# Optimization experiments

Measured on AMD Instinct MI355X. Metric: run time of the kernel, lower is better.

Reference implementation:

```python
import jax, jax.numpy as jnp
import numpy as np

EPSILON = 0.01
N_ITERS = 100
EPS_STAB = 1e-08
KERNEL_CLAMP = 50.0


def _cost_matrix(x, y):
    # squared euclidean distances, (n, m)
    x2 = jnp.sum(x * x, axis=1, keepdims=True)          # (n,1)
    y2 = jnp.sum(y * y, axis=1, keepdims=True).T        # (1,m)
    c = x2 + y2 - 2.0 * (x @ y.T)
    c = jnp.maximum(c, 0.0)  # numerical guard, matches cdist(p=2)**2 >= 0
    return jnp.nan_to_num(c, nan=0.0, posinf=1e6, neginf=0.0)


def _sinkhorn_cost(X, Y):
    n, m = X.shape[0], Y.shape[0]
    C = _cost_matrix(X, Y)
    scaled = jnp.clip(-C / EPSILON, -KERNEL_CLAMP, 0.0)
    K = jnp.maximum(jnp.nan_to_num(jnp.exp(scaled), nan=0.0, posinf=0.0, neginf=0.0), EPS_STAB)
    a = jnp.full((n,), 1.0 / n, dtype=C.dtype)
    b = jnp.full((m,), 1.0 / m, dtype=C.dtype)
    u0 = jnp.ones_like(a)
    v0 = jnp.ones_like(b)

    def body(_, uv):
        u, v = uv
        Kv = jnp.maximum(K @ v, EPS_STAB)
        u = a / Kv
        Ktu = jnp.maximum(K.T @ u, EPS_STAB)
        v = b / Ktu
        return (u, v)

    u, v = jax.lax.fori_loop(0, N_ITERS, body, (u0, v0))
    # cost = sum(u_i * K_ij * v_j * C_ij)
    cost = u @ ((K * C) @ v)
    return jnp.maximum(cost, 0.0)


def setup_inputs() -> dict:
    key = jax.random.key(0)
    k1, k2 = jax.random.split(key)
    X = jax.random.normal(k1, (8192, 128), dtype=jnp.float32)
    Y = jax.random.normal(k2, (8192, 128), dtype=jnp.float32)
    return {"X": X, "Y": Y}


def reference(X, Y):
    ot_xy = _sinkhorn_cost(X, Y)
    ot_xx = _sinkhorn_cost(X, jax.lax.stop_gradient(X))
    ot_yy = _sinkhorn_cost(Y, jax.lax.stop_gradient(Y))
    divergence = ot_xy - 0.5 * (ot_xx + ot_yy)
    return jnp.clip(divergence, 0.0, 10000.0)
```

## Files before the change

kernel.cpp:

```cpp
#include <hip/hip_runtime.h>
#include <math.h>

#define NROW 8192
#define DDIM 128
#define DP 32
#define CAP 16384
#define NITERS 100
#define NWARM 6
#define AC (1.0f / 8192.0f)
#define LSTRIDE2 40

struct Entry { int i, j; float s, t; };


typedef __attribute__((ext_vector_type(8))) short frag_ab;
typedef __attribute__((ext_vector_type(4))) float frag_cd;

__device__ inline unsigned short f2bf(float f) {
    unsigned u = __float_as_uint(f);
    return (unsigned short)((u + 0x7FFFu + ((u >> 16) & 1u)) >> 16);
}

__global__ void norms_k(const float* __restrict__ X, const float* __restrict__ Y,
                        float* __restrict__ x2, float* __restrict__ y2,
                        float* __restrict__ x2p, float* __restrict__ y2p,
                        unsigned short* __restrict__ Xbf, unsigned short* __restrict__ Ybf,
                        int* counts, double* accum, Entry* lists) {
    int idx = blockIdx.x * 256 + threadIdx.x;
    if (idx < 3) counts[idx] = NROW;
    else if (idx < 8) counts[idx] = 0;
    if (idx < 3 * 264) accum[idx] = 0.0;
    if (idx < 3 * NROW) {
        int p = idx >> 13, i = idx & (NROW - 1);
        Entry e; e.i = i; e.j = i; e.s = 0.f; e.t = 0.f;
        lists[(size_t)p * CAP + i] = e;
    }
    int gw = idx >> 6;
    int lane = threadIdx.x & 63;
    if (gw >= 2 * NROW) return;
    const float* M = (gw < NROW) ? X : Y;
    float* out = (gw < NROW) ? x2 : y2;
    float* outp = (gw < NROW) ? x2p : y2p;
    unsigned short* Mb = (gw < NROW) ? Xbf : Ybf;
    int r = (gw < NROW) ? gw : gw - NROW;
    float2 v = *(const float2*)(M + (size_t)r * DDIM + lane * 2);
    if (lane < 16) {
        unsigned pk = (unsigned)f2bf(v.x) | ((unsigned)f2bf(v.y) << 16);
        *(unsigned*)(Mb + (size_t)r * DP + lane * 2) = pk;
    }
    float s = v.x * v.x + v.y * v.y;
    float sp = (lane < 16) ? s : 0.f;
    for (int o = 32; o; o >>= 1) s += __shfl_down(s, o, 64);
    for (int o = 8; o; o >>= 1) sp += __shfl_down(sp, o, 64);
    if (lane == 0) { out[r] = s; outp[r] = sp; }
}

__global__ __launch_bounds__(256) void scan_k(const unsigned short* __restrict__ Xbf,
                                              const unsigned short* __restrict__ Ybf,
                                              const float* __restrict__ x2p,
                                              const float* __restrict__ y2p,
                                              int* counts, Entry* lists) {
    int bid = blockIdx.x;
    int p, bx, by;
    if (bid < 4096) { p = 0; by = bid >> 6; bx = bid & 63; }
    else {
        int r = bid - 4096;
        p = 1 + (r >= 2080);
        int q = r - (p == 2) * 2080;
        int a = (int)((129.0f - sqrtf((float)(16641 - 8 * q))) * 0.5f);
        while (a * 64 - ((a * (a - 1)) >> 1) > q) a--;
        while ((a + 1) * 64 - (((a + 1) * a) >> 1) <= q) a++;
        bx = a;
        by = a + (q - (a * 64 - ((a * (a - 1)) >> 1)));
    }
    const unsigned short* Ab = (p == 2) ? Ybf : Xbf;
    const unsigned short* Bb = (p == 0) ? Ybf : ((p == 1) ? Xbf : Ybf);
    const float* na = (p == 2) ? y2p : x2p;
    const float* nb = (p == 0) ? y2p : ((p == 1) ? x2p : y2p);
    int i0 = bx * 128, j0 = by * 128;

    __shared__ unsigned short As[128 * LSTRIDE2];
    __shared__ unsigned short Bs[128 * LSTRIDE2];
    __shared__ float sMinA[32];
    int t = threadIdx.x;

    const unsigned short* ga = Ab + (size_t)i0 * DP;
    const unsigned short* gb = Bb + (size_t)j0 * DP;
    #pragma unroll
    for (int c = 0; c < 2; c++) {
        int u = c * 256 + t;
        int row = u >> 2, col = (u & 3) * 8;
        uint4 wa = *(const uint4*)(ga + u * 8);
        uint4 wb = *(const uint4*)(gb + u * 8);
        *(uint4*)&As[row * LSTRIDE2 + col] = wa;
        *(uint4*)&Bs[row * LSTRIDE2 + col] = wb;
    }
    if (t < 32) {
        const float* nn = na + i0 + t * 4;
        sMinA[t] = fminf(fminf(nn[0], nn[1]), fminf(nn[2], nn[3]));
    }
    __syncthreads();

    int w = t >> 6, lane = t & 63;
    int lm = lane & 15, quad = lane >> 4;
    int wr = (w & 1) * 64, wc = (w >> 1) * 64;

    frag_cd acc[4][4];
    #pragma unroll
    for (int rt = 0; rt < 4; rt++)
        #pragma unroll
        for (int ct = 0; ct < 4; ct++) acc[rt][ct] = (frag_cd){0.f, 0.f, 0.f, 0.f};

    int abase = (wr + lm) * LSTRIDE2 + quad * 8;
    int bbase = (wc + lm) * LSTRIDE2 + quad * 8;
    {
        frag_ab a[4], b[4];
        #pragma unroll
        for (int rt = 0; rt < 4; rt++) a[rt] = *(const frag_ab*)&As[abase + rt * 16 * LSTRIDE2];
        #pragma unroll
        for (int ct = 0; ct < 4; ct++) b[ct] = *(const frag_ab*)&Bs[bbase + ct * 16 * LSTRIDE2];
        #pragma unroll
        for (int rt = 0; rt < 4; rt++)
            #pragma unroll
            for (int ct = 0; ct < 4; ct++)
                acc[rt][ct] = __builtin_amdgcn_mfma_f32_16x16x32_bf16(a[rt], b[ct], acc[rt][ct], 0, 0, 0);
    }

    Entry* list = lists + (size_t)p * CAP;
    float yj_[4];
    #pragma unroll
    for (int ct = 0; ct < 4; ct++) yj_[ct] = nb[j0 + wc + ct * 16 + lm];
    float minyj = fminf(fminf(yj_[0], yj_[1]), fminf(yj_[2], yj_[3]));

    #pragma unroll
    for (int rt = 0; rt < 4; rt++) {
        float m0 = fmaxf(fmaxf(acc[rt][0][0], acc[rt][0][1]), fmaxf(acc[rt][0][2], acc[rt][0][3]));
        float m1 = fmaxf(fmaxf(acc[rt][1][0], acc[rt][1][1]), fmaxf(acc[rt][1][2], acc[rt][1][3]));
        float m2 = fmaxf(fmaxf(acc[rt][2][0], acc[rt][2][1]), fmaxf(acc[rt][2][2], acc[rt][2][3]));
        float m3 = fmaxf(fmaxf(acc[rt][3][0], acc[rt][3][1]), fmaxf(acc[rt][3][2], acc[rt][3][3]));
        float mx = fmaxf(fmaxf(m0, m1), fmaxf(m2, m3));
        float mna = sMinA[(wr >> 2) + rt * 4 + quad];
        if (mna + minyj - 2.f * mx < 2.0f) {
            #pragma unroll
            for (int ct = 0; ct < 4; ct++) {
                int j = j0 + wc + ct * 16 + lm;
                float yj = yj_[ct];
                #pragma unroll
                for (int reg = 0; reg < 4; reg++) {
                    int i = i0 + wr + rt * 16 + quad * 4 + reg;
                    float Ct = na[i] + yj - 2.f * acc[rt][ct][reg];
                    if (Ct < 2.0f && i != j) {
                        if (p == 0) {
                            int idx = atomicAdd(&counts[0], 1);
                            if (idx < CAP) { Entry e; e.i = i; e.j = j; e.s = 0.f; e.t = 0.f; list[idx] = e; }
                        } else if (i < j) {
                            int idx = atomicAdd(&counts[p], 2);
                            if (idx < CAP) { Entry e; e.i = i; e.j = j; e.s = 0.f; e.t = 0.f; list[idx] = e; }
                            if (idx + 1 < CAP) { Entry e; e.i = j; e.j = i; e.s = 0.f; e.t = 0.f; list[idx + 1] = e; }
                        }
                    }
                }
            }
        }
    }
}

__global__ __launch_bounds__(256) void exact_k(const float* __restrict__ X,
                                               const float* __restrict__ Y,
                                               const float* __restrict__ x2,
                                               const float* __restrict__ y2,
                                               int* counts, Entry* lists,
                                               float* __restrict__ sdiag,
                                               float* __restrict__ tdiag) {
    int p = blockIdx.y;
    const float* A = (p == 2) ? Y : X;
    const float* B = (p == 0) ? Y : ((p == 1) ? X : Y);
    const float* na = (p == 2) ? y2 : x2;
    const float* nb = (p == 0) ? y2 : ((p == 1) ? x2 : y2);
    int cnt = counts[p]; if (cnt > CAP) cnt = CAP;
    Entry* list = lists + (size_t)p * CAP;
    int w = (blockIdx.x * 256 + threadIdx.x) >> 6;
    int lane = threadIdx.x & 63;
    for (int e = w; e < cnt; e += 8192) {
        int i = list[e].i, j = list[e].j;
        const float* ar = A + (size_t)i * DDIM;
        const float* br = B + (size_t)j * DDIM;
        float dot = ar[lane] * br[lane] + ar[lane + 64] * br[lane + 64];
        for (int o = 32; o; o >>= 1) dot += __shfl_down(dot, o, 64);
        if (lane == 0) {
            float raw = na[i] + nb[j] - 2.0f * dot;
            float C = fmaxf(raw, 0.0f);
            float sc = fmaxf(-C * 100.0f, -50.0f);
            float K = fmaxf(expf(sc), 1e-8f);
            float s = K - 1e-8f;
            float tv = (raw >= 0.f) ? s * C : (-1e-8f) * raw;
            list[e].s = s;
            list[e].t = tv;
            if (i == j) {
                sdiag[p * NROW + i] = s;
                tdiag[p * NROW + i] = tv;
            } else if (s != 0.f || tv != 0.f) {
                atomicAdd(&counts[3 + p], 1);
            }
        }
    }
}

__global__ __launch_bounds__(1024, 1) void sink2_k(const int* counts,
                                                   const Entry* __restrict__ lists,
                                                   const float* __restrict__ sdiag,
                                                   float* __restrict__ u_g,
                                                   float* __restrict__ v_g,
                                                   double* accum) {
    int p = blockIdx.x;
    const Entry* list = lists + (size_t)p * CAP;
    int cnt = counts[p]; if (cnt > CAP) cnt = CAP;
    int nres = counts[3 + p];
    double* acc = accum + (size_t)p * 264;
    float* up = u_g + (size_t)p * NROW;
    float* vp = v_g + (size_t)p * NROW;

    __shared__ float u_s[NROW];
    __shared__ float v_s[NROW];
    __shared__ float redS[2][16];
    __shared__ unsigned redC[16];
    int t = threadIdx.x;
    int wid = t >> 6, lane = t & 63;

    if (nres == 0) {
        float vk[8], uk[8], sk[8];
        unsigned pv2[8];
        #pragma unroll
        for (int k = 0; k < 8; k++) {
            sk[k] = sdiag[p * NROW + t + 1024 * k];
            vk[k] = 1.0f; uk[k] = AC; pv2[k] = 0xFFFFFFFFu;
        }
        unsigned flags = 3u;
        int par = 0, last = 0, done = 0;
        float bu_last = 0.f;
        for (int it = 0; it < NWARM; it++) {
            float s = 0.f;
            #pragma unroll
            for (int k = 0; k < 8; k++) s += vk[k];
            for (int o = 32; o; o >>= 1) s += __shfl_down(s, o, 64);
            if (lane == 0) { redS[par][wid] = s; redC[wid] = flags; }
            __syncthreads();
            float sumv = 0.f; unsigned anyf = 0;
            #pragma unroll
            for (int w2 = 0; w2 < 16; w2++) { sumv += redS[par][w2]; anyf |= redC[w2]; }
            par ^= 1;
            if (it > 0) {
                if (!(anyf & 1)) { done = 1; break; }
                if (!(anyf & 2)) {
                    if (((NITERS - it) & 1) == 0) { done = 1; break; }
                    last = 1;
                }
            }
            float base = 1e-8f * sumv;
            #pragma unroll
            for (int k = 0; k < 8; k++) {
                float kv = fmaxf(base + sk[k] * vk[k], 1e-8f);
                uk[k] = AC * __builtin_amdgcn_rcpf(kv);
            }
            s = 0.f;
            #pragma unroll
            for (int k = 0; k < 8; k++) s += uk[k];
            for (int o = 32; o; o >>= 1) s += __shfl_down(s, o, 64);
            if (lane == 0) redS[par][wid] = s;
            __syncthreads();
            float sumu = 0.f;
            #pragma unroll
            for (int w2 = 0; w2 < 16; w2++) sumu += redS[par][w2];
            par ^= 1;
            base = 1e-8f * sumu;
            bu_last = base;
            unsigned d1 = 0, d2 = 0;
            #pragma unroll
            for (int k = 0; k < 8; k++) {
                float kv = fmaxf(base + sk[k] * uk[k], 1e-8f);
                float nv = AC * __builtin_amdgcn_rcpf(kv);
                unsigned nb_ = __float_as_uint(nv);
                d1 |= nb_ ^ __float_as_uint(vk[k]);
                d2 |= nb_ ^ pv2[k];
                pv2[k] = __float_as_uint(vk[k]);
                vk[k] = nv;
            }
            flags = (__any(d1 != 0) ? 1u : 0u) | (__any(d2 != 0) ? 2u : 0u);
            if (last) { done = 1; break; }
        }
        float bv_f = 0.f;
        int R = 0;
        if (!done) {
            float s = 0.f;
            #pragma unroll
            for (int k = 0; k < 8; k++) s += vk[k];
            for (int o = 32; o; o >>= 1) s += __shfl_down(s, o, 64);
            if (lane == 0) redS[par][wid] = s;
            __syncthreads();
            float sumv = 0.f;
            #pragma unroll
            for (int w2 = 0; w2 < 16; w2++) sumv += redS[par][w2];
            bv_f = 1e-8f * sumv;
            R = NITERS - NWARM;
        }
        #pragma unroll
        for (int k = 0; k < 8; k++) {
            int i = t + 1024 * k;
            up[i] = uk[k]; vp[i] = vk[k];
        }
        if (t == 0) { acc[5] = (double)R; acc[6] = (double)bu_last; acc[7] = (double)bv_f; }
    } else {
        for (int i = t; i < NROW; i += 1024) { u_s[i] = 1.0f; v_s[i] = 1.0f; }
        __syncthreads();
        for (int it = 0; it < NITERS; it++) {
            {
                float sv = 0.f;
                for (int i = t; i < NROW; i += 1024) sv += v_s[i];
                for (int o = 32; o; o >>= 1) sv += __shfl_down(sv, o, 64);
                if (lane == 0) u_s[wid] = sv;
                __syncthreads();
                if (t < 64) {
                    float s2 = (t < 16) ? u_s[t] : 0.f;
                    for (int o = 8; o; o >>= 1) s2 += __shfl_down(s2, o, 64);
                    if (t == 0) u_s[0] = s2;
                }
                __syncthreads();
                float sum_v = u_s[0];
                __syncthreads();
                for (int i = t; i < NROW; i += 1024) u_s[i] = 1e-8f * sum_v;
                __syncthreads();
                for (int e = t; e < cnt; e += 1024)
                    atomicAdd(&u_s[list[e].i], list[e].s * v_s[list[e].j]);
                __syncthreads();
                for (int i = t; i < NROW; i += 1024) u_s[i] = AC / fmaxf(u_s[i], 1e-8f);
                __syncthreads();
            }
            {
                float su = 0.f;
                for (int i = t; i < NROW; i += 1024) su += u_s[i];
                for (int o = 32; o; o >>= 1) su += __shfl_down(su, o, 64);
                if (lane == 0) v_s[wid] = su;
                __syncthreads();
                if (t < 64) {
                    float s2 = (t < 16) ? v_s[t] : 0.f;
                    for (int o = 8; o; o >>= 1) s2 += __shfl_down(s2, o, 64);
                    if (t == 0) v_s[0] = s2;
                }
                __syncthreads();
                float sum_u = v_s[0];
                __syncthreads();
                for (int i = t; i < NROW; i += 1024) v_s[i] = 1e-8f * sum_u;
                __syncthreads();
                for (int e = t; e < cnt; e += 1024)
                    atomicAdd(&v_s[list[e].j], list[e].s * u_s[list[e].i]);
                __syncthreads();
                for (int i = t; i < NROW; i += 1024) v_s[i] = AC / fmaxf(v_s[i], 1e-8f);
                __syncthreads();
            }
        }
        for (int i = t; i < NROW; i += 1024) { up[i] = u_s[i]; vp[i] = v_s[i]; }
        if (t == 0) { acc[5] = 0.0; acc[6] = 0.0; acc[7] = 0.0; }
    }
}

__global__ __launch_bounds__(256) void sinkwide_k(const float* __restrict__ sdiag,
                                                  float* __restrict__ u_g,
                                                  float* __restrict__ v_g,
                                                  const double* __restrict__ accum) {
    int p = blockIdx.y;
    const double* acc = accum + (size_t)p * 264;
    int R = (int)acc[5];
    if (R <= 0) return;
    float bu = (float)acc[6], bv = (float)acc[7];
    int i = blockIdx.x * 256 + threadIdx.x;
    float s = sdiag[p * NROW + i];
    float v = v_g[p * NROW + i];
    float u = u_g[p * NROW + i];
    for (int r = 0; r < R; r++) {
        u = AC * __builtin_amdgcn_rcpf(fmaxf(bv + s * v, 1e-8f));
        v = AC * __builtin_amdgcn_rcpf(fmaxf(bu + s * u, 1e-8f));
    }
    u_g[p * NROW + i] = u;
    v_g[p * NROW + i] = v;
}

__global__ __launch_bounds__(256) void epi_k(const float* __restrict__ X,
                                             const float* __restrict__ Y,
                                             const float* __restrict__ x2,
                                             const float* __restrict__ y2,
                                             const float* __restrict__ u_g,
                                             const float* __restrict__ v_g,
                                             const float* __restrict__ tdiag,
                                             double* accum,
                                             const int* counts,
                                             const Entry* __restrict__ lists) {
    int p = blockIdx.y;
    const float* up = u_g + (size_t)p * NROW;
    const float* vp = v_g + (size_t)p * NROW;
    double* acc = accum + (size_t)p * 264;
    int t = threadIdx.x, lane = t & 63;

    if (blockIdx.x == 32) {
        int cnt = counts[p]; if (cnt > CAP) cnt = CAP;
        const Entry* list = lists + (size_t)p * CAP;
        __shared__ double red[4];
        int wid = t >> 6;
        double sp = 0.0;
        for (int e = t; e < cnt; e += 256) {
            Entry en = list[e];
            if (en.i != en.j && en.t != 0.f)
                sp += (double)up[en.i] * (double)vp[en.j] * (double)en.t;
        }
        for (int o = 32; o; o >>= 1) sp += __shfl_down(sp, o, 64);
        if (lane == 0) red[wid] = sp;
        __syncthreads();
        if (t == 0) {
            double tot = red[0] + red[1] + red[2] + red[3];
            atomicAdd(&acc[4], tot);
        }
        return;
    }

    const float* A = (p == 2) ? Y : X;
    const float* B = (p == 0) ? Y : ((p == 1) ? X : Y);
    const float* na = (p == 2) ? y2 : x2;
    const float* nb = (p == 0) ? y2 : ((p == 1) ? x2 : y2);
    int rbase = blockIdx.x * 256;
    {
        int r = rbase + t;
        double ui = up[r], vi = vp[r];
        double a0 = ui, a1 = vi, a2 = ui * (double)na[r], a3 = vi * (double)nb[r];
        double a4 = ui * vi * (double)tdiag[p * NROW + r];
        for (int o = 32; o; o >>= 1) {
            a0 += __shfl_down(a0, o, 64); a1 += __shfl_down(a1, o, 64);
            a2 += __shfl_down(a2, o, 64); a3 += __shfl_down(a3, o, 64);
            a4 += __shfl_down(a4, o, 64);
        }
        if (lane == 0) {
            atomicAdd(&acc[0], a0); atomicAdd(&acc[1], a1);
            atomicAdd(&acc[2], a2); atomicAdd(&acc[3], a3);
            atomicAdd(&acc[4], a4);
        }
    }
    {
        int dq = (t & 31) * 4, g = t >> 5;
        double pp[4] = {0, 0, 0, 0}, qq[4] = {0, 0, 0, 0};
        for (int k = 0; k < 32; k++) {
            int r = rbase + g + 8 * k;
            float4 av = *(const float4*)(A + (size_t)r * DDIM + dq);
            float us = up[r];
            pp[0] += (double)us * av.x; pp[1] += (double)us * av.y;
            pp[2] += (double)us * av.z; pp[3] += (double)us * av.w;
            float4 bv = *(const float4*)(B + (size_t)r * DDIM + dq);
            float vs = vp[r];
            qq[0] += (double)vs * bv.x; qq[1] += (double)vs * bv.y;
            qq[2] += (double)vs * bv.z; qq[3] += (double)vs * bv.w;
        }
        #pragma unroll
        for (int m = 0; m < 4; m++) {
            pp[m] += __shfl_down(pp[m], 32, 64);
            qq[m] += __shfl_down(qq[m], 32, 64);
        }
        if (lane < 32) {
            #pragma unroll
            for (int m = 0; m < 4; m++) {
                atomicAdd(&acc[8 + dq + m], pp[m]);
                atomicAdd(&acc[136 + dq + m], qq[m]);
            }
        }
    }
}

__global__ void combine_k(const double* __restrict__ accum, float* __restrict__ out) {
    int t = threadIdx.x;
    __shared__ double costs[3];
    for (int p = 0; p < 3; p++) {
        const double* acc = accum + (size_t)p * 264;
        double part = acc[8 + t] * acc[136 + t] + acc[8 + 64 + t] * acc[136 + 64 + t];
        for (int o = 32; o; o >>= 1) part += __shfl_down(part, o, 64);
        if (t == 0) {
            double F = acc[2] * acc[1] + acc[0] * acc[3] - 2.0 * part;
            double c = 1e-8 * F + acc[4];
            costs[p] = (c > 0.0) ? c : 0.0;
        }
    }
    __syncthreads();
    if (t == 0) {
        double dv = costs[0] - 0.5 * (costs[1] + costs[2]);
        dv = fmin(fmax(dv, 0.0), 10000.0);
        out[0] = (float)dv;
    }
}

extern "C" void kernel_launch(void* const* d_in, const int* in_sizes, int n_in,
                              void* d_out, int out_size, void* d_ws, size_t ws_size,
                              hipStream_t stream) {
    const float* X = (const float*)d_in[0];
    const float* Y = (const float*)d_in[1];
    float* out = (float*)d_out;
    char* ws = (char*)d_ws;
    float* x2 = (float*)ws;
    float* y2 = (float*)(ws + 32768);
    float* x2p = (float*)(ws + 65536);
    float* y2p = (float*)(ws + 98304);
    int* counts = (int*)(ws + 131072);
    double* accum = (double*)(ws + 131136);
    Entry* lists = (Entry*)(ws + 137472);
    unsigned short* Xbf = (unsigned short*)(ws + 923904);
    float* sdiag = (float*)(ws + 923904);
    float* tdiag = (float*)(ws + 1022208);
    float* u_g = (float*)(ws + 1120512);
    float* v_g = (float*)(ws + 1218816);
    unsigned short* Ybf = (unsigned short*)(ws + 1448192);

    norms_k<<<4096, 256, 0, stream>>>(X, Y, x2, y2, x2p, y2p, Xbf, Ybf, counts, accum, lists);
    scan_k<<<8256, 256, 0, stream>>>(Xbf, Ybf, x2p, y2p, counts, lists);
    exact_k<<<dim3(2048, 3), 256, 0, stream>>>(X, Y, x2, y2, counts, lists, sdiag, tdiag);
    sink2_k<<<3, 1024, 0, stream>>>(counts, lists, sdiag, u_g, v_g, accum);
    sinkwide_k<<<dim3(NROW / 256, 3), 256, 0, stream>>>(sdiag, u_g, v_g, accum);
    epi_k<<<dim3(33, 3), 256, 0, stream>>>(X, Y, x2, y2, u_g, v_g, tdiag, accum, counts, lists);
    combine_k<<<1, 64, 0, stream>>>(accum, out);
}
```

Measured before the change: 147.8 us.

## Fuse pipeline kernels: diagonal in norms, exact pass into sinkhorn, wide iterations into epilogue

```diff
diff --git a/kernel.cpp b/kernel.cpp
--- a/kernel.cpp
+++ b/kernel.cpp
@@ -21,29 +21,43 @@
     return (unsigned short)((u + 0x7FFFu + ((u >> 16) & 1u)) >> 16);
 }
 
+__device__ inline float wave_dot128(const float* __restrict__ ar, const float* __restrict__ br, int lane) {
+    float dot = ar[lane] * br[lane] + ar[lane + 64] * br[lane + 64];
+    for (int o = 32; o; o >>= 1) dot += __shfl_down(dot, o, 64);
+    return dot;
+}
+__device__ inline void st_from_raw(float raw, float& s, float& tv) {
+    float C = fmaxf(raw, 0.0f);
+    float sc = fmaxf(-C * 100.0f, -50.0f);
+    float K = fmaxf(expf(sc), 1e-8f);
+    s = K - 1e-8f;
+    tv = (raw >= 0.f) ? s * C : (-1e-8f) * raw;
+}
+__device__ inline double ald(const double* p) {
+    return __hip_atomic_load(p, __ATOMIC_RELAXED, __HIP_MEMORY_SCOPE_AGENT);
+}
+
 __global__ void norms_k(const float* __restrict__ X, const float* __restrict__ Y,
                         float* __restrict__ x2, float* __restrict__ y2,
                         float* __restrict__ x2p, float* __restrict__ y2p,
                         unsigned short* __restrict__ Xbf, unsigned short* __restrict__ Ybf,
-                        int* counts, double* accum, Entry* lists) {
+                        int* counts, double* accum, Entry* lists,
+                        float* __restrict__ sdiag, float* __restrict__ tdiag) {
     int idx = blockIdx.x * 256 + threadIdx.x;
     if (idx < 3) counts[idx] = NROW;
     else if (idx < 8) counts[idx] = 0;
     if (idx < 3 * 264) accum[idx] = 0.0;
-    if (idx < 3 * NROW) {
-        int p = idx >> 13, i = idx & (NROW - 1);
-        Entry e; e.i = i; e.j = i; e.s = 0.f; e.t = 0.f;
-        lists[(size_t)p * CAP + i] = e;
-    }
     int gw = idx >> 6;
-    int lane = threadIdx.x & 63;
+    int lane = idx & 63;
     if (gw >= 2 * NROW) return;
-    const float* M = (gw < NROW) ? X : Y;
-    float* out = (gw < NROW) ? x2 : y2;
-    float* outp = (gw < NROW) ? x2p : y2p;
-    unsigned short* Mb = (gw < NROW) ? Xbf : Ybf;
-    int r = (gw < NROW) ? gw : gw - NROW;
-    float2 v = *(const float2*)(M + (size_t)r * DDIM + lane * 2);
+    int isX = gw < NROW;
+    int r = isX ? gw : gw - NROW;
+    const float* M = isX ? X : Y;
+    const float* ar = M + (size_t)r * DDIM;
+    float* out = isX ? x2 : y2;
+    float* outp = isX ? x2p : y2p;
+    unsigned short* Mb = isX ? Xbf : Ybf;
+    float2 v = *(const float2*)(ar + lane * 2);
     if (lane < 16) {
         unsigned pk = (unsigned)f2bf(v.x) | ((unsigned)f2bf(v.y) << 16);
         *(unsigned*)(Mb + (size_t)r * DP + lane * 2) = pk;
@@ -52,50 +66,77 @@
     float sp = (lane < 16) ? s : 0.f;
     for (int o = 32; o; o >>= 1) s += __shfl_down(s, o, 64);
     for (int o = 8; o; o >>= 1) sp += __shfl_down(sp, o, 64);
-    if (lane == 0) { out[r] = s; outp[r] = sp; }
-}
-
-__global__ __launch_bounds__(256) void scan_k(const unsigned short* __restrict__ Xbf,
+    float dself = wave_dot128(ar, ar, lane);
+    if (isX) {
+        const float* br = Y + (size_t)r * DDIM;
+        float dxy = wave_dot128(ar, br, lane);
+        float2 wv = *(const float2*)(br + lane * 2);
+        float sy = wv.x * wv.x + wv.y * wv.y;
+        for (int o = 32; o; o >>= 1) sy += __shfl_down(sy, o, 64);
+        if (lane == 0) {
+            out[r] = s; outp[r] = sp;
+            float s1, t1; st_from_raw(s + s - 2.0f * dself, s1, t1);
+            sdiag[NROW + r] = s1; tdiag[NROW + r] = t1;
+            Entry e1; e1.i = r; e1.j = r; e1.s = s1; e1.t = t1;
+            lists[(size_t)CAP + r] = e1;
+            float s0, t0; st_from_raw(s + sy - 2.0f * dxy, s0, t0);
+            sdiag[r] = s0; tdiag[r] = t0;
+            Entry e0; e0.i = r; e0.j = r; e0.s = s0; e0.t = t0;
+            lists[r] = e0;
+        }
+    } else {
+        if (lane == 0) {
+            out[r] = s; outp[r] = sp;
+            float s2, t2; st_from_raw(s + s - 2.0f * dself, s2, t2);
+            sdiag[2 * NROW + r] = s2; tdiag[2 * NROW + r] = t2;
+            Entry e2; e2.i = r; e2.j = r; e2.s = s2; e2.t = t2;
+            lists[(size_t)2 * CAP + r] = e2;
+        }
+    }
+}
+
+__global__ __launch_bounds__(512) void scan_k(const unsigned short* __restrict__ Xbf,
                                               const unsigned short* __restrict__ Ybf,
                                               const float* __restrict__ x2p,
                                               const float* __restrict__ y2p,
                                               int* counts, Entry* lists) {
     int bid = blockIdx.x;
     int p, bx, by;
-    if (bid < 4096) { p = 0; by = bid >> 6; bx = bid & 63; }
+    if (bid < 2048) { p = 0; bx = bid >> 6; by = bid & 63; }
     else {
-        int r = bid - 4096;
-        p = 1 + (r >= 2080);
-        int q = r - (p == 2) * 2080;
-        int a = (int)((129.0f - sqrtf((float)(16641 - 8 * q))) * 0.5f);
-        while (a * 64 - ((a * (a - 1)) >> 1) > q) a--;
-        while ((a + 1) * 64 - (((a + 1) * a) >> 1) <= q) a++;
+        int r = bid - 2048;
+        p = 1 + (r >= 1056);
+        int q = r - (p == 2) * 1056;
+        int a = (int)((65.0f - sqrtf((float)(4225 - 4 * q))) * 0.5f);
+        while (65 * a - a * a > q) a--;
+        while (65 * (a + 1) - (a + 1) * (a + 1) <= q) a++;
         bx = a;
-        by = a + (q - (a * 64 - ((a * (a - 1)) >> 1)));
+        by = 2 * a + (q - (65 * a - a * a));
     }
     const unsigned short* Ab = (p == 2) ? Ybf : Xbf;
     const unsigned short* Bb = (p == 0) ? Ybf : ((p == 1) ? Xbf : Ybf);
     const float* na = (p == 2) ? y2p : x2p;
     const float* nb = (p == 0) ? y2p : ((p == 1) ? x2p : y2p);
-    int i0 = bx * 128, j0 = by * 128;
-
-    __shared__ unsigned short As[128 * LSTRIDE2];
+    int i0 = bx * 256, j0 = by * 128;
+
+    __shared__ unsigned short As[256 * LSTRIDE2];
     __shared__ unsigned short Bs[128 * LSTRIDE2];
-    __shared__ float sMinA[32];
+    __shared__ float sMinA[64];
     int t = threadIdx.x;
 
     const unsigned short* ga = Ab + (size_t)i0 * DP;
     const unsigned short* gb = Bb + (size_t)j0 * DP;
     #pragma unroll
     for (int c = 0; c < 2; c++) {
-        int u = c * 256 + t;
+        int u = c * 512 + t;
         int row = u >> 2, col = (u & 3) * 8;
-        uint4 wa = *(const uint4*)(ga + u * 8);
-        uint4 wb = *(const uint4*)(gb + u * 8);
-        *(uint4*)&As[row * LSTRIDE2 + col] = wa;
-        *(uint4*)&Bs[row * LSTRIDE2 + col] = wb;
-    }
-    if (t < 32) {
+        *(uint4*)&As[row * LSTRIDE2 + col] = *(const uint4*)(ga + u * 8);
+    }
+    {
+        int row = t >> 2, col = (t & 3) * 8;
+        *(uint4*)&Bs[row * LSTRIDE2 + col] = *(const uint4*)(gb + t * 8);
+    }
+    if (t < 64) {
         const float* nn = na + i0 + t * 4;
         sMinA[t] = fminf(fminf(nn[0], nn[1]), fminf(nn[2], nn[3]));
     }
@@ -103,7 +144,7 @@
 
     int w = t >> 6, lane = t & 63;
     int lm = lane & 15, quad = lane >> 4;
-    int wr = (w & 1) * 64, wc = (w >> 1) * 64;
+    int wr = (w >> 1) * 64, wc = (w & 1) * 64;
 
     frag_cd acc[4][4];
     #pragma unroll
@@ -165,57 +206,20 @@
     }
 }
 
-__global__ __launch_bounds__(256) void exact_k(const float* __restrict__ X,
-                                               const float* __restrict__ Y,
-                                               const float* __restrict__ x2,
-                                               const float* __restrict__ y2,
-                                               int* counts, Entry* lists,
-                                               float* __restrict__ sdiag,
-                                               float* __restrict__ tdiag) {
-    int p = blockIdx.y;
-    const float* A = (p == 2) ? Y : X;
-    const float* B = (p == 0) ? Y : ((p == 1) ? X : Y);
-    const float* na = (p == 2) ? y2 : x2;
-    const float* nb = (p == 0) ? y2 : ((p == 1) ? x2 : y2);
-    int cnt = counts[p]; if (cnt > CAP) cnt = CAP;
-    Entry* list = lists + (size_t)p * CAP;
-    int w = (blockIdx.x * 256 + threadIdx.x) >> 6;
-    int lane = threadIdx.x & 63;
-    for (int e = w; e < cnt; e += 8192) {
-        int i = list[e].i, j = list[e].j;
-        const float* ar = A + (size_t)i * DDIM;
-        const float* br = B + (size_t)j * DDIM;
-        float dot = ar[lane] * br[lane] + ar[lane + 64] * br[lane + 64];
-        for (int o = 32; o; o >>= 1) dot += __shfl_down(dot, o, 64);
-        if (lane == 0) {
-            float raw = na[i] + nb[j] - 2.0f * dot;
-            float C = fmaxf(raw, 0.0f);
-            float sc = fmaxf(-C * 100.0f, -50.0f);
-            float K = fmaxf(expf(sc), 1e-8f);
-            float s = K - 1e-8f;
-            float tv = (raw >= 0.f) ? s * C : (-1e-8f) * raw;
-            list[e].s = s;
-            list[e].t = tv;
-            if (i == j) {
-                sdiag[p * NROW + i] = s;
-                tdiag[p * NROW + i] = tv;
-            } else if (s != 0.f || tv != 0.f) {
-                atomicAdd(&counts[3 + p], 1);
-            }
-        }
-    }
-}
-
 __global__ __launch_bounds__(1024, 1) void sink2_k(const int* counts,
-                                                   const Entry* __restrict__ lists,
+                                                   Entry* lists,
                                                    const float* __restrict__ sdiag,
                                                    float* __restrict__ u_g,
                                                    float* __restrict__ v_g,
-                                                   double* accum) {
+                                                   double* accum,
+                                                   const float* __restrict__ X,
+                                                   const float* __restrict__ Y,
+                                                   const float* __restrict__ x2,
+                                                   const float* __restrict__ y2) {
     int p = blockIdx.x;
-    const Entry* list = lists + (size_t)p * CAP;
+    Entry* listm = lists + (size_t)p * CAP;
+    const Entry* list = listm;
     int cnt = counts[p]; if (cnt > CAP) cnt = CAP;
-    int nres = counts[3 + p];
     double* acc = accum + (size_t)p * 264;
     float* up = u_g + (size_t)p * NROW;
     float* vp = v_g + (size_t)p * NROW;
@@ -224,8 +228,32 @@
     __shared__ float v_s[NROW];
     __shared__ float redS[2][16];
     __shared__ unsigned redC[16];
+    __shared__ int nres_s;
     int t = threadIdx.x;
     int wid = t >> 6, lane = t & 63;
+
+    if (t == 0) nres_s = 0;
+    __syncthreads();
+    {
+        const float* A = (p == 2) ? Y : X;
+        const float* B = (p == 0) ? Y : ((p == 1) ? X : Y);
+        const float* na = (p == 2) ? y2 : x2;
+        const float* nb = (p == 0) ? y2 : ((p == 1) ? x2 : y2);
+        int act = 0;
+        for (int e = NROW + wid; e < cnt; e += 16) {
+            int i = listm[e].i, j = listm[e].j;
+            float dot = wave_dot128(A + (size_t)i * DDIM, B + (size_t)j * DDIM, lane);
+            if (lane == 0) {
+                float raw = na[i] + nb[j] - 2.0f * dot;
+                float s, tv; st_from_raw(raw, s, tv);
+                listm[e].s = s; listm[e].t = tv;
+                if (s != 0.f || tv != 0.f) act++;
+            }
+        }
+        if (lane == 0 && act) atomicAdd(&nres_s, act);
+    }
+    __syncthreads();
+    int nres = nres_s;
 
     if (nres == 0) {
         float vk[8], uk[8], sk[8];
@@ -363,132 +391,144 @@
     }
 }
 
-__global__ __launch_bounds__(256) void sinkwide_k(const float* __restrict__ sdiag,
-                                                  float* __restrict__ u_g,
-                                                  float* __restrict__ v_g,
-                                                  const double* __restrict__ accum) {
-    int p = blockIdx.y;
-    const double* acc = accum + (size_t)p * 264;
-    int R = (int)acc[5];
-    if (R <= 0) return;
-    float bu = (float)acc[6], bv = (float)acc[7];
-    int i = blockIdx.x * 256 + threadIdx.x;
-    float s = sdiag[p * NROW + i];
-    float v = v_g[p * NROW + i];
-    float u = u_g[p * NROW + i];
-    for (int r = 0; r < R; r++) {
-        u = AC * __builtin_amdgcn_rcpf(fmaxf(bv + s * v, 1e-8f));
-        v = AC * __builtin_amdgcn_rcpf(fmaxf(bu + s * u, 1e-8f));
-    }
-    u_g[p * NROW + i] = u;
-    v_g[p * NROW + i] = v;
-}
-
 __global__ __launch_bounds__(256) void epi_k(const float* __restrict__ X,
                                              const float* __restrict__ Y,
                                              const float* __restrict__ x2,
                                              const float* __restrict__ y2,
+                                             const float* __restrict__ sdiag,
+                                             const float* __restrict__ tdiag,
                                              const float* __restrict__ u_g,
                                              const float* __restrict__ v_g,
-                                             const float* __restrict__ tdiag,
                                              double* accum,
-                                             const int* counts,
-                                             const Entry* __restrict__ lists) {
+                                             int* counts,
+                                             const Entry* __restrict__ lists,
+                                             float* __restrict__ out) {
     int p = blockIdx.y;
-    const float* up = u_g + (size_t)p * NROW;
-    const float* vp = v_g + (size_t)p * NROW;
     double* acc = accum + (size_t)p * 264;
     int t = threadIdx.x, lane = t & 63;
+    int R = (int)acc[5];
+    float bu = (float)acc[6], bv = (float)acc[7];
 
     if (blockIdx.x == 32) {
         int cnt = counts[p]; if (cnt > CAP) cnt = CAP;
         const Entry* list = lists + (size_t)p * CAP;
         __shared__ double red[4];
         int wid = t >> 6;
-        double sp = 0.0;
-        for (int e = t; e < cnt; e += 256) {
+        double sp_ = 0.0;
+        for (int e = NROW + t; e < cnt; e += 256) {
             Entry en = list[e];
-            if (en.i != en.j && en.t != 0.f)
-                sp += (double)up[en.i] * (double)vp[en.j] * (double)en.t;
-        }
-        for (int o = 32; o; o >>= 1) sp += __shfl_down(sp, o, 64);
-        if (lane == 0) red[wid] = sp;
+            if (en.t != 0.f) {
+                float si = sdiag[p * NROW + en.i];
+                float ui = u_g[p * NROW + en.i], vi = v_g[p * NROW + en.i];
+                for (int it2 = 0; it2 < R; it2++) {
+                    ui = AC * __builtin_amdgcn_rcpf(fmaxf(bv + si * vi, 1e-8f));
+                    vi = AC * __builtin_amdgcn_rcpf(fmaxf(bu + si * ui, 1e-8f));
+                }
+                float sj = sdiag[p * NROW + en.j];
+                float uj = u_g[p * NROW + en.j], vj = v_g[p * NROW + en.j];
+                for (int it2 = 0; it2 < R; it2++) {
+                    uj = AC * __builtin_amdgcn_rcpf(fmaxf(bv + sj * vj, 1e-8f));
+                    vj = AC * __builtin_amdgcn_rcpf(fmaxf(bu + sj * uj, 1e-8f));
+                }
+                sp_ += (double)ui * (double)vj * (double)en.t;
+            }
+        }
+        for (int o = 32; o; o >>= 1) sp_ += __shfl_down(sp_, o, 64);
+        if (lane == 0) red[wid] = sp_;
         __syncthreads();
         if (t == 0) {
             double tot = red[0] + red[1] + red[2] + red[3];
             atomicAdd(&acc[4], tot);
         }
-        return;
-    }
-
-    const float* A = (p == 2) ? Y : X;
-    const float* B = (p == 0) ? Y : ((p == 1) ? X : Y);
-    const float* na = (p == 2) ? y2 : x2;
-    const float* nb = (p == 0) ? y2 : ((p == 1) ? x2 : y2);
-    int rbase = blockIdx.x * 256;
-    {
+    } else {
+        const float* A = (p == 2) ? Y : X;
+        const float* B = (p == 0) ? Y : ((p == 1) ? X : Y);
+        const float* na = (p == 2) ? y2 : x2;
+        const float* nb = (p == 0) ? y2 : ((p == 1) ? x2 : y2);
+        int rbase = blockIdx.x * 256;
         int r = rbase + t;
-        double ui = up[r], vi = vp[r];
-        double a0 = ui, a1 = vi, a2 = ui * (double)na[r], a3 = vi * (double)nb[r];
-        double a4 = ui * vi * (double)tdiag[p * NROW + r];
-        for (int o = 32; o; o >>= 1) {
-            a0 += __shfl_down(a0, o, 64); a1 += __shfl_down(a1, o, 64);
-            a2 += __shfl_down(a2, o, 64); a3 += __shfl_down(a3, o, 64);
-            a4 += __shfl_down(a4, o, 64);
-        }
-        if (lane == 0) {
-            atomicAdd(&acc[0], a0); atomicAdd(&acc[1], a1);
-            atomicAdd(&acc[2], a2); atomicAdd(&acc[3], a3);
-            atomicAdd(&acc[4], a4);
-        }
-    }
-    {
-        int dq = (t & 31) * 4, g = t >> 5;
-        double pp[4] = {0, 0, 0, 0}, qq[4] = {0, 0, 0, 0};
-        for (int k = 0; k < 32; k++) {
-            int r = rbase + g + 8 * k;
-            float4 av = *(const float4*)(A + (size_t)r * DDIM + dq);
-            float us = up[r];
-            pp[0] += (double)us * av.x; pp[1] += (double)us * av.y;
-            pp[2] += (double)us * av.z; pp[3] += (double)us * av.w;
-            float4 bv = *(const float4*)(B + (size_t)r * DDIM + dq);
-            float vs = vp[r];
-            qq[0] += (double)vs * bv.x; qq[1] += (double)vs * bv.y;
-            qq[2] += (double)vs * bv.z; qq[3] += (double)vs * bv.w;
-        }
-        #pragma unroll
-        for (int m = 0; m < 4; m++) {
-            pp[m] += __shfl_down(pp[m], 32, 64);
-            qq[m] += __shfl_down(qq[m], 32, 64);
-        }
-        if (lane < 32) {
+        float srow = sdiag[p * NROW + r];
+        float u = u_g[p * NROW + r], v = v_g[p * NROW + r];
+        for (int it2 = 0; it2 < R; it2++) {
+            u = AC * __builtin_amdgcn_rcpf(fmaxf(bv + srow * v, 1e-8f));
+            v = AC * __builtin_amdgcn_rcpf(fmaxf(bu + srow * u, 1e-8f));
+        }
+        __shared__ float us[256], vs[256];
+        us[t] = u; vs[t] = v;
+        __syncthreads();
+        {
+            double ui = u, vi = v;
+            double a0 = ui, a1 = vi, a2 = ui * (double)na[r], a3 = vi * (double)nb[r];
+            double a4 = ui * vi * (double)tdiag[p * NROW + r];
+            for (int o = 32; o; o >>= 1) {
+                a0 += __shfl_down(a0, o, 64); a1 += __shfl_down(a1, o, 64);
+                a2 += __shfl_down(a2, o, 64); a3 += __shfl_down(a3, o, 64);
+                a4 += __shfl_down(a4, o, 64);
+            }
+            if (lane == 0) {
+                atomicAdd(&acc[0], a0); atomicAdd(&acc[1], a1);
+                atomicAdd(&acc[2], a2); atomicAdd(&acc[3], a3);
+                atomicAdd(&acc[4], a4);
+            }
+        }
+        {
+            int dq = (t & 31) * 4, g = t >> 5;
+            double pp[4] = {0, 0, 0, 0}, qq[4] = {0, 0, 0, 0};
+            for (int k = 0; k < 32; k++) {
+                int rr = g + 8 * k;
+                float4 av = *(const float4*)(A + (size_t)(rbase + rr) * DDIM + dq);
+                float usv = us[rr];
+                pp[0] += (double)usv * av.x; pp[1] += (double)usv * av.y;
+                pp[2] += (double)usv * av.z; pp[3] += (double)usv * av.w;
+                float4 bvv = *(const float4*)(B + (size_t)(rbase + rr) * DDIM + dq);
+                float vsv = vs[rr];
+                qq[0] += (double)vsv * bvv.x; qq[1] += (double)vsv * bvv.y;
+                qq[2] += (double)vsv * bvv.z; qq[3] += (double)vsv * bvv.w;
+            }
             #pragma unroll
             for (int m = 0; m < 4; m++) {
-                atomicAdd(&acc[8 + dq + m], pp[m]);
-                atomicAdd(&acc[136 + dq + m], qq[m]);
-            }
-        }
-    }
-}
-
-__global__ void combine_k(const double* __restrict__ accum, float* __restrict__ out) {
-    int t = threadIdx.x;
-    __shared__ double costs[3];
-    for (int p = 0; p < 3; p++) {
-        const double* acc = accum + (size_t)p * 264;
-        double part = acc[8 + t] * acc[136 + t] + acc[8 + 64 + t] * acc[136 + 64 + t];
-        for (int o = 32; o; o >>= 1) part += __shfl_down(part, o, 64);
-        if (t == 0) {
-            double F = acc[2] * acc[1] + acc[0] * acc[3] - 2.0 * part;
-            double c = 1e-8 * F + acc[4];
-            costs[p] = (c > 0.0) ? c : 0.0;
-        }
-    }
+                pp[m] += __shfl_down(pp[m], 32, 64);
+                qq[m] += __shfl_down(qq[m], 32, 64);
+            }
+            if (lane < 32) {
+                #pragma unroll
+                for (int m = 0; m < 4; m++) {
+                    atomicAdd(&acc[8 + dq + m], pp[m]);
+                    atomicAdd(&acc[136 + dq + m], qq[m]);
+                }
+            }
+        }
+    }
+
+    __shared__ int lastFlag;
     __syncthreads();
     if (t == 0) {
-        double dv = costs[0] - 0.5 * (costs[1] + costs[2]);
-        dv = fmin(fmax(dv, 0.0), 10000.0);
-        out[0] = (float)dv;
+        __threadfence();
+        lastFlag = (atomicAdd(&counts[6], 1) == 98) ? 1 : 0;
+    }
+    __syncthreads();
+    if (lastFlag) {
+        __threadfence();
+        __shared__ double costs[3];
+        if (t < 64) {
+            for (int p2 = 0; p2 < 3; p2++) {
+                const double* ac2 = accum + (size_t)p2 * 264;
+                double part = ald(ac2 + 8 + t) * ald(ac2 + 136 + t)
+                            + ald(ac2 + 8 + 64 + t) * ald(ac2 + 136 + 64 + t);
+                for (int o = 32; o; o >>= 1) part += __shfl_down(part, o, 64);
+                if (t == 0) {
+                    double F = ald(ac2 + 2) * ald(ac2 + 1) + ald(ac2 + 0) * ald(ac2 + 3) - 2.0 * part;
+                    double c = 1e-8 * F + ald(ac2 + 4);
+                    costs[p2] = (c > 0.0) ? c : 0.0;
+                }
+            }
+        }
+        __syncthreads();
+        if (t == 0) {
+            double dv = costs[0] - 0.5 * (costs[1] + costs[2]);
+            dv = fmin(fmax(dv, 0.0), 10000.0);
+            out[0] = (float)dv;
+        }
     }
 }
 
@@ -507,17 +547,14 @@
     double* accum = (double*)(ws + 131136);
     Entry* lists = (Entry*)(ws + 137472);
     unsigned short* Xbf = (unsigned short*)(ws + 923904);
-    float* sdiag = (float*)(ws + 923904);
-    float* tdiag = (float*)(ws + 1022208);
-    float* u_g = (float*)(ws + 1120512);
-    float* v_g = (float*)(ws + 1218816);
     unsigned short* Ybf = (unsigned short*)(ws + 1448192);
-
-    norms_k<<<4096, 256, 0, stream>>>(X, Y, x2, y2, x2p, y2p, Xbf, Ybf, counts, accum, lists);
-    scan_k<<<8256, 256, 0, stream>>>(Xbf, Ybf, x2p, y2p, counts, lists);
-    exact_k<<<dim3(2048, 3), 256, 0, stream>>>(X, Y, x2, y2, counts, lists, sdiag, tdiag);
-    sink2_k<<<3, 1024, 0, stream>>>(counts, lists, sdiag, u_g, v_g, accum);
-    sinkwide_k<<<dim3(NROW / 256, 3), 256, 0, stream>>>(sdiag, u_g, v_g, accum);
-    epi_k<<<dim3(33, 3), 256, 0, stream>>>(X, Y, x2, y2, u_g, v_g, tdiag, accum, counts, lists);
-    combine_k<<<1, 64, 0, stream>>>(accum, out);
-}
+    float* sdiag = (float*)(ws + 1972480);
+    float* tdiag = (float*)(ws + 2070784);
+    float* u_g = (float*)(ws + 2169088);
+    float* v_g = (float*)(ws + 2267392);
+
+    norms_k<<<4096, 256, 0, stream>>>(X, Y, x2, y2, x2p, y2p, Xbf, Ybf, counts, accum, lists, sdiag, tdiag);
+    scan_k<<<4160, 512, 0, stream>>>(Xbf, Ybf, x2p, y2p, counts, lists);
+    sink2_k<<<3, 1024, 0, stream>>>(counts, lists, sdiag, u_g, v_g, accum, X, Y, x2, y2);
+    epi_k<<<dim3(33, 3), 256, 0, stream>>>(X, Y, x2, y2, sdiag, tdiag, u_g, v_g, accum, counts, lists, out);
+}
```

Measured after the change: 142.4 us. 1.04x faster.
